# Kernel optimization log

Hardware: AMD Instinct MI355X
Metric: run time of the kernel (lower is better)

Reference implementation:

```python
import jax, jax.numpy as jnp
import numpy as np

F_SIZE = 256
N_HEAD = 4
D_HEAD = F_SIZE // N_HEAD
B = 16384
E = 31  # number of 'other' entities


def setup_inputs() -> dict:
    key = jax.random.key(0)
    ks = jax.random.split(key, 9)
    s = 1.0 / np.sqrt(F_SIZE)  # ~ nn.Linear init scale
    inp = {
        "ego": jax.random.normal(ks[0], (B, 1, F_SIZE), dtype=jnp.float32),
        "others": jax.random.normal(ks[1], (B, E, F_SIZE), dtype=jnp.float32),
        "mask": jax.random.randint(ks[2], (B, E + 1), 0, 2).astype(bool),
        "Wq": jax.random.uniform(ks[3], (F_SIZE, F_SIZE), jnp.float32, -s, s),
        "Wk": jax.random.uniform(ks[4], (F_SIZE, F_SIZE), jnp.float32, -s, s),
        "Wv": jax.random.uniform(ks[5], (F_SIZE, F_SIZE), jnp.float32, -s, s),
        "Wok": jax.random.uniform(ks[6], (F_SIZE, F_SIZE), jnp.float32, -s, s),
        "Wov": jax.random.uniform(ks[7], (F_SIZE, F_SIZE), jnp.float32, -s, s),
        "Wc": jax.random.uniform(ks[8], (F_SIZE, F_SIZE), jnp.float32, -s, s),
    }
    return inp


def reference(ego, others, mask, Wq, Wk, Wv, Wok, Wov, Wc):
    b = others.shape[0]
    e = others.shape[1]
    # nn.Linear(bias=False): y = x @ W.T
    ego_q = (ego @ Wq.T).reshape(b, 1, N_HEAD, D_HEAD)
    ego_k = (ego @ Wk.T).reshape(b, 1, N_HEAD, D_HEAD)
    ego_v = (ego @ Wv.T).reshape(b, 1, N_HEAD, D_HEAD)
    oth_k = (others @ Wok.T).reshape(b, e, N_HEAD, D_HEAD)
    oth_v = (others @ Wov.T).reshape(b, e, N_HEAD, D_HEAD)
    all_k = jnp.concatenate([ego_k, oth_k], axis=1)  # (b, e+1, h, d)
    all_v = jnp.concatenate([ego_v, oth_v], axis=1)
    # scores: single query per head -> (b, h, 1, e+1)
    scores = jnp.einsum('bqhd,bkhd->bhqk', ego_q, all_k) / np.sqrt(D_HEAD)
    scores = jnp.where(mask[:, None, None, :], jnp.float32(-1e9), scores)
    attn = jax.nn.softmax(scores, axis=-1)
    value = jnp.einsum('bhqk,bkhd->bqhd', attn, all_v).reshape(b, F_SIZE)
    res = ((value @ Wc.T) + ego[:, 0, :]) * 0.5
    return res, attn
```

## Files before the change

### kernel.cpp

```cpp
#include <hip/hip_runtime.h>
#include <hip/hip_bf16.h>

typedef __attribute__((ext_vector_type(8))) short bf16x8;
typedef __attribute__((ext_vector_type(4))) float f32x4;

#define NB 16384
#define NE 31

static __device__ __forceinline__ unsigned short f2b(float f) {
  unsigned int u = __builtin_bit_cast(unsigned int, f);
  return (unsigned short)((u + 0x7fffu + ((u >> 16) & 1u)) >> 16);
}
static __device__ __forceinline__ float b2f(unsigned short h) {
  return __builtin_bit_cast(float, ((unsigned int)h) << 16);
}


__global__ void k0_base(const float* __restrict__ wq, const float* __restrict__ wk,
                        const float* __restrict__ wv, const float* __restrict__ wc,
                        unsigned short* __restrict__ W1, unsigned short* __restrict__ W2) {
  int r = blockIdx.x, k = threadIdx.x;
  if (r < 256) {
    W1[r * 256 + k] = f2b(0.125f * wq[r * 256 + k]);
  } else if (r < 512) {
    W1[r * 256 + k] = f2b(wk[(r - 256) * 256 + k]);
  } else if (r < 768) {
    W1[r * 256 + k] = f2b(wv[(r - 512) * 256 + k]);
  } else {
    int n = r - 768;
    W2[n * 1280 + 1024 + k] = f2b(wc[n * 256 + k]);
  }
}

__global__ void k0_wqo(const float* __restrict__ wq, const float* __restrict__ wok,
                       unsigned short* __restrict__ W1) {
  int m = blockIdx.x;
  int k = threadIdx.x;
  int h = m >> 8, c = m & 255;
  float acc = 0.f;
#pragma unroll 8
  for (int d = 0; d < 64; ++d)
    acc = fmaf(wq[(h * 64 + d) * 256 + k], wok[(h * 64 + d) * 256 + c], acc);
  W1[(768 + m) * 256 + k] = f2b(0.125f * acc);
}

__global__ void k0_g(const float* __restrict__ wov, const float* __restrict__ wc,
                     unsigned short* __restrict__ W2) {
  int n = blockIdx.x;
  int t = threadIdx.x;
#pragma unroll 1
  for (int mi = 0; mi < 4; ++mi) {
    float acc = 0.f;
#pragma unroll 8
    for (int d = 0; d < 64; ++d)
      acc = fmaf(wov[(mi * 64 + d) * 256 + t], wc[n * 256 + mi * 64 + d], acc);
    W2[n * 1280 + mi * 256 + t] = f2b(acc);
  }
}

__global__ __launch_bounds__(256, 2)
void k1b(const float* __restrict__ ego, const unsigned short* __restrict__ W1,
         unsigned short* __restrict__ qkv2) {
  __shared__ __align__(16) unsigned short Al[64 * 256];
  const int tid = threadIdx.x;
  const int bM = blockIdx.x * 64;
#pragma unroll
  for (int it = 0; it < 8; ++it) {
    int c = tid + it * 256;
    int row = c >> 5, k8 = c & 31;
    const float4* g = (const float4*)(ego + (size_t)(bM + row) * 256 + k8 * 8);
    float4 x = g[0], y = g[1];
    float t[8] = {x.x, x.y, x.z, x.w, y.x, y.y, y.z, y.w};
    bf16x8 v;
#pragma unroll
    for (int j = 0; j < 8; ++j) v[j] = (short)f2b(t[j]);
    int byteoff = row * 512 + ((k8 * 16) ^ ((row & 7) << 4));
    *(bf16x8*)((char*)Al + byteoff) = v;
  }
  __syncthreads();
  const int w = tid >> 6, lane = tid & 63, lr = lane & 15, lkg = lane >> 4;
#pragma unroll 1
  for (int cb = 0; cb < 7; ++cb) {
    int bN = w * 448 + cb * 64;
    f32x4 acc[4][4];
#pragma unroll
    for (int mt = 0; mt < 4; ++mt)
#pragma unroll
      for (int nt = 0; nt < 4; ++nt) acc[mt][nt] = (f32x4){0.f, 0.f, 0.f, 0.f};
#pragma unroll
    for (int kk = 0; kk < 8; ++kk) {
      int kidx = kk * 32 + lkg * 8;
      bf16x8 bfr[4];
#pragma unroll
      for (int nt = 0; nt < 4; ++nt)
        bfr[nt] = *(const bf16x8*)(W1 + (size_t)(bN + nt * 16 + lr) * 256 + kidx);
#pragma unroll
      for (int mt = 0; mt < 4; ++mt) {
        int row = mt * 16 + lr;
        int byteoff = row * 512 + ((kidx * 2) ^ ((row & 7) << 4));
        bf16x8 a = *(const bf16x8*)((const char*)Al + byteoff);
#pragma unroll
        for (int nt = 0; nt < 4; ++nt)
          acc[mt][nt] = __builtin_amdgcn_mfma_f32_16x16x32_bf16(a, bfr[nt], acc[mt][nt], 0, 0, 0);
      }
    }
#pragma unroll
    for (int mt = 0; mt < 4; ++mt)
#pragma unroll
      for (int nt = 0; nt < 4; ++nt)
#pragma unroll
        for (int j = 0; j < 4; ++j) {
          int row = bM + mt * 16 + lkg * 4 + j;
          int col = bN + nt * 16 + lr;
          qkv2[(size_t)row * 1792 + col] = f2b(acc[mt][nt][j]);
        }
  }
}

__global__ __launch_bounds__(256, 4)
void ks_attn(const float* __restrict__ others, const int* __restrict__ mask,
             const unsigned short* __restrict__ qkv2,
             unsigned short* __restrict__ u,
             float* __restrict__ attnout) {
  __shared__ __align__(16) unsigned short Xr[32 * 264];
  __shared__ __align__(16) unsigned short Qo_l[1024];
  __shared__ __align__(16) unsigned short qk_l[768];
  __shared__ float sco_l[4][32];
  __shared__ float Pl[4][32];
  const int tid = threadIdx.x;
  const size_t b = blockIdx.x;

  {
    int e = tid >> 3, c = tid & 7;
    if (e < 31) {
      const float4* src = (const float4*)(others) + ((b * 31 + e) * 64 + c * 8);
      float4 f[8];
#pragma unroll
      for (int j = 0; j < 8; ++j) f[j] = src[j];
#pragma unroll
      for (int j = 0; j < 4; ++j) {
        bf16x8 v;
        v[0] = (short)f2b(f[2 * j].x);     v[1] = (short)f2b(f[2 * j].y);
        v[2] = (short)f2b(f[2 * j].z);     v[3] = (short)f2b(f[2 * j].w);
        v[4] = (short)f2b(f[2 * j + 1].x); v[5] = (short)f2b(f[2 * j + 1].y);
        v[6] = (short)f2b(f[2 * j + 1].z); v[7] = (short)f2b(f[2 * j + 1].w);
        *(bf16x8*)(&Xr[e * 264 + c * 32 + j * 8]) = v;
      }
    } else {
      bf16x8 z = (bf16x8){0, 0, 0, 0, 0, 0, 0, 0};
#pragma unroll
      for (int j = 0; j < 4; ++j) *(bf16x8*)(&Xr[31 * 264 + c * 32 + j * 8]) = z;
    }
    if (tid < 224) {
      bf16x8 v = *(const bf16x8*)(qkv2 + b * 1792 + tid * 8);
      if (tid < 96) *(bf16x8*)(&qk_l[tid * 8]) = v;
      else          *(bf16x8*)(&Qo_l[(tid - 96) * 8]) = v;
    }
  }
  __syncthreads();

  const int w = tid >> 6, lane = tid & 63, lr = lane & 15, lkg = lane >> 4;

  if (w < 2) {
    f32x4 acc = (f32x4){0.f, 0.f, 0.f, 0.f};
#pragma unroll
    for (int kk = 0; kk < 8; ++kk) {
      bf16x8 a = *(const bf16x8*)(&Qo_l[(lr & 3) * 256 + kk * 32 + lkg * 8]);
      bf16x8 bb = *(const bf16x8*)(&Xr[(w * 16 + lr) * 264 + kk * 32 + lkg * 8]);
      acc = __builtin_amdgcn_mfma_f32_16x16x32_bf16(a, bb, acc, 0, 0, 0);
    }
    if (lkg == 0) {
      int n = w * 16 + lr;
      if (n < NE) {
#pragma unroll
        for (int j = 0; j < 4; ++j) sco_l[j][1 + n] = acc[j];
      }
    }
  } else if (w == 2) {
    int h = lane >> 4, i = lane & 15;
    const unsigned short* q4 = &qk_l[h * 64 + i * 4];
    const unsigned short* k4p = &qk_l[256 + h * 64 + i * 4];
    float s = 0.f;
#pragma unroll
    for (int j = 0; j < 4; ++j) s += b2f(q4[j]) * b2f(k4p[j]);
#pragma unroll
    for (int off = 1; off < 16; off <<= 1) s += __shfl_xor(s, off, 16);
    if (i == 0) sco_l[h][0] = s;
  }
  __syncthreads();

  {
    int key = lane & 31;
    float s = sco_l[w][key];
    if (mask[b * 32 + key] != 0) s = -1e9f;
    float mx = s;
#pragma unroll
    for (int off = 1; off < 32; off <<= 1) mx = fmaxf(mx, __shfl_xor(mx, off, 32));
    float ex = __expf(s - mx);
    float sm = ex;
#pragma unroll
    for (int off = 1; off < 32; off <<= 1) sm += __shfl_xor(sm, off, 32);
    float p = ex / sm;
    if (lane < 32) {
      Pl[w][key] = p;
      attnout[b * 128 + w * 32 + key] = p;
    }
  }

  {
    float a0 = 0.f, a1 = 0.f, a2 = 0.f, a3 = 0.f;
#pragma unroll
    for (int e = 0; e < NE; ++e) {
      float p = Pl[w][1 + e];
      ushort4 xv = *(const ushort4*)(&Xr[e * 264 + lane * 4]);
      a0 = fmaf(p, b2f(xv.x), a0);
      a1 = fmaf(p, b2f(xv.y), a1);
      a2 = fmaf(p, b2f(xv.z), a2);
      a3 = fmaf(p, b2f(xv.w), a3);
    }
    ushort4 st;
    st.x = f2b(a0); st.y = f2b(a1); st.z = f2b(a2); st.w = f2b(a3);
    *(ushort4*)(u + b * 1280 + w * 256 + lane * 4) = st;
    float p0 = Pl[w][0];
    u[b * 1280 + 1024 + w * 64 + lane] = f2b(p0 * b2f(qk_l[512 + w * 64 + lane]));
  }
}

__global__ __launch_bounds__(256, 2)
void k4_out(const unsigned short* __restrict__ u, const unsigned short* __restrict__ W2,
            const float* __restrict__ ego, float* __restrict__ out) {
  __shared__ __align__(16) unsigned short Au[32 * 256];
  const int tid = threadIdx.x;
  const int bM = blockIdx.x * 32;
  const int w = tid >> 6, lane = tid & 63, lr = lane & 15, lkg = lane >> 4;
  f32x4 acc[2][4];
#pragma unroll
  for (int mt = 0; mt < 2; ++mt)
#pragma unroll
    for (int nt = 0; nt < 4; ++nt) acc[mt][nt] = (f32x4){0.f, 0.f, 0.f, 0.f};
#pragma unroll 1
  for (int kc = 0; kc < 5; ++kc) {
#pragma unroll
    for (int it = 0; it < 4; ++it) {
      int c = tid + it * 256;
      int row = c >> 5, k8 = c & 31;
      bf16x8 v = *(const bf16x8*)(u + (size_t)(bM + row) * 1280 + kc * 256 + k8 * 8);
      int byteoff = row * 512 + ((k8 * 16) ^ ((row & 7) << 4));
      *(bf16x8*)((char*)Au + byteoff) = v;
    }
    __syncthreads();
#pragma unroll
    for (int kk = 0; kk < 8; ++kk) {
      int kidx = kk * 32 + lkg * 8;
      bf16x8 bfr[4];
#pragma unroll
      for (int nt = 0; nt < 4; ++nt)
        bfr[nt] = *(const bf16x8*)(W2 + (size_t)(w * 64 + nt * 16 + lr) * 1280 + kc * 256 + kidx);
#pragma unroll
      for (int mt = 0; mt < 2; ++mt) {
        int row = mt * 16 + lr;
        int byteoff = row * 512 + ((kidx * 2) ^ ((row & 7) << 4));
        bf16x8 a = *(const bf16x8*)((const char*)Au + byteoff);
#pragma unroll
        for (int nt = 0; nt < 4; ++nt)
          acc[mt][nt] = __builtin_amdgcn_mfma_f32_16x16x32_bf16(a, bfr[nt], acc[mt][nt], 0, 0, 0);
      }
    }
    __syncthreads();
  }
#pragma unroll
  for (int mt = 0; mt < 2; ++mt)
#pragma unroll
    for (int nt = 0; nt < 4; ++nt)
#pragma unroll
      for (int j = 0; j < 4; ++j) {
        int row = bM + mt * 16 + lkg * 4 + j;
        int col = w * 64 + nt * 16 + lr;
        out[(size_t)row * 256 + col] = (acc[mt][nt][j] + ego[(size_t)row * 256 + col]) * 0.5f;
      }
}

extern "C" void kernel_launch(void* const* d_in, const int* in_sizes, int n_in,
                              void* d_out, int out_size, void* d_ws, size_t ws_size,
                              hipStream_t stream) {
  const float* ego    = (const float*)d_in[0];
  const float* others = (const float*)d_in[1];
  const int*   mask   = (const int*)d_in[2];
  const float* wq  = (const float*)d_in[3];
  const float* wk  = (const float*)d_in[4];
  const float* wv  = (const float*)d_in[5];
  const float* wok = (const float*)d_in[6];
  const float* wov = (const float*)d_in[7];
  const float* wc  = (const float*)d_in[8];

  unsigned short* W1   = (unsigned short*)d_ws;
  unsigned short* W2   = W1 + 1792 * 256;
  unsigned short* qkv2 = W2 + 256 * 1280;
  unsigned short* u    = qkv2 + (size_t)NB * 1792;

  float* res  = (float*)d_out;
  float* attn = res + (size_t)NB * 256;

  hipLaunchKernelGGL(k0_base, dim3(1024), dim3(256), 0, stream, wq, wk, wv, wc, W1, W2);
  hipLaunchKernelGGL(k0_wqo,  dim3(1024), dim3(256), 0, stream, wq, wok, W1);
  hipLaunchKernelGGL(k0_g,    dim3(256),  dim3(256), 0, stream, wov, wc, W2);
  hipLaunchKernelGGL(k1b,     dim3(256),  dim3(256), 0, stream, ego, W1, qkv2);
  hipLaunchKernelGGL(ks_attn, dim3(NB),   dim3(256), 0, stream, others, mask, qkv2, u, attn);
  hipLaunchKernelGGL(k4_out,  dim3(512),  dim3(256), 0, stream, u, W2, ego, res);
}
```

Baseline: 268.1 us.

## Make attention kernel persistent with register-prefetched next batch and merge weight-prep kernels

The attention kernel now runs on a fixed grid of 1024 blocks. Each block loops over 16 batch rows and issues global loads for the next row into registers while computing the current one. The mask is staged in shared memory, and the three weight-preparation kernels are merged into one launch. The aim is to hide the global-load latency of the dominant memory-bound kernel and to cut launch overhead. In exchange, register pressure rises from holding the prefetch buffers, each iteration needs an extra barrier, and fewer blocks are resident to hide latency.

```diff
diff --git a/kernel.cpp b/kernel.cpp
--- a/kernel.cpp
+++ b/kernel.cpp
@@ -6,6 +6,8 @@
 
 #define NB 16384
 #define NE 31
+#define KS_GRID 1024
+#define KS_ITEMS (NB / KS_GRID)
 
 static __device__ __forceinline__ unsigned short f2b(float f) {
   unsigned int u = __builtin_bit_cast(unsigned int, f);
@@ -15,46 +17,40 @@
   return __builtin_bit_cast(float, ((unsigned int)h) << 16);
 }
 
-
-__global__ void k0_base(const float* __restrict__ wq, const float* __restrict__ wk,
-                        const float* __restrict__ wv, const float* __restrict__ wc,
-                        unsigned short* __restrict__ W1, unsigned short* __restrict__ W2) {
+__global__ void k0_all(const float* __restrict__ wq, const float* __restrict__ wk,
+                       const float* __restrict__ wv, const float* __restrict__ wok,
+                       const float* __restrict__ wov, const float* __restrict__ wc,
+                       unsigned short* __restrict__ W1, unsigned short* __restrict__ W2) {
   int r = blockIdx.x, k = threadIdx.x;
-  if (r < 256) {
-    W1[r * 256 + k] = f2b(0.125f * wq[r * 256 + k]);
-  } else if (r < 512) {
-    W1[r * 256 + k] = f2b(wk[(r - 256) * 256 + k]);
-  } else if (r < 768) {
-    W1[r * 256 + k] = f2b(wv[(r - 512) * 256 + k]);
-  } else {
-    int n = r - 768;
-    W2[n * 1280 + 1024 + k] = f2b(wc[n * 256 + k]);
-  }
-}
-
-__global__ void k0_wqo(const float* __restrict__ wq, const float* __restrict__ wok,
-                       unsigned short* __restrict__ W1) {
-  int m = blockIdx.x;
-  int k = threadIdx.x;
-  int h = m >> 8, c = m & 255;
-  float acc = 0.f;
-#pragma unroll 8
-  for (int d = 0; d < 64; ++d)
-    acc = fmaf(wq[(h * 64 + d) * 256 + k], wok[(h * 64 + d) * 256 + c], acc);
-  W1[(768 + m) * 256 + k] = f2b(0.125f * acc);
-}
-
-__global__ void k0_g(const float* __restrict__ wov, const float* __restrict__ wc,
-                     unsigned short* __restrict__ W2) {
-  int n = blockIdx.x;
-  int t = threadIdx.x;
-#pragma unroll 1
-  for (int mi = 0; mi < 4; ++mi) {
+  if (r < 1024) {
+    if (r < 256) {
+      W1[r * 256 + k] = f2b(0.125f * wq[r * 256 + k]);
+    } else if (r < 512) {
+      W1[r * 256 + k] = f2b(wk[(r - 256) * 256 + k]);
+    } else if (r < 768) {
+      W1[r * 256 + k] = f2b(wv[(r - 512) * 256 + k]);
+    } else {
+      int n = r - 768;
+      W2[n * 1280 + 1024 + k] = f2b(wc[n * 256 + k]);
+    }
+  } else if (r < 2048) {
+    int m = r - 1024;
+    int h = m >> 8, c = m & 255;
     float acc = 0.f;
 #pragma unroll 8
     for (int d = 0; d < 64; ++d)
-      acc = fmaf(wov[(mi * 64 + d) * 256 + t], wc[n * 256 + mi * 64 + d], acc);
-    W2[n * 1280 + mi * 256 + t] = f2b(acc);
+      acc = fmaf(wq[(h * 64 + d) * 256 + k], wok[(h * 64 + d) * 256 + c], acc);
+    W1[(768 + m) * 256 + k] = f2b(0.125f * acc);
+  } else {
+    int n = r - 2048;
+#pragma unroll 1
+    for (int mi = 0; mi < 4; ++mi) {
+      float acc = 0.f;
+#pragma unroll 8
+      for (int d = 0; d < 64; ++d)
+        acc = fmaf(wov[(mi * 64 + d) * 256 + k], wc[n * 256 + mi * 64 + d], acc);
+      W2[n * 1280 + mi * 256 + k] = f2b(acc);
+    }
   }
 }
 
@@ -125,18 +121,29 @@
   __shared__ __align__(16) unsigned short Xr[32 * 264];
   __shared__ __align__(16) unsigned short Qo_l[1024];
   __shared__ __align__(16) unsigned short qk_l[768];
+  __shared__ int maskl[32];
   __shared__ float sco_l[4][32];
   __shared__ float Pl[4][32];
   const int tid = threadIdx.x;
-  const size_t b = blockIdx.x;
-
-  {
-    int e = tid >> 3, c = tid & 7;
+  const int w = tid >> 6, lane = tid & 63, lr = lane & 15, lkg = lane >> 4;
+  const int e = tid >> 3, c = tid & 7;
+  const size_t b0 = (size_t)blockIdx.x * KS_ITEMS;
+
+  float4 f[8];
+  bf16x8 qv;
+  int4 mv;
+
+  auto issue = [&](size_t bb) {
     if (e < 31) {
-      const float4* src = (const float4*)(others) + ((b * 31 + e) * 64 + c * 8);
-      float4 f[8];
+      const float4* src = (const float4*)(others) + ((bb * 31 + e) * 64 + c * 8);
 #pragma unroll
       for (int j = 0; j < 8; ++j) f[j] = src[j];
+    }
+    if (tid < 224) qv = *(const bf16x8*)(qkv2 + bb * 1792 + tid * 8);
+    if (tid >= 248) mv = *(const int4*)(mask + bb * 32 + (tid - 248) * 4);
+  };
+  auto commit = [&]() {
+    if (e < 31) {
 #pragma unroll
       for (int j = 0; j < 4; ++j) {
         bf16x8 v;
@@ -150,79 +157,90 @@
       bf16x8 z = (bf16x8){0, 0, 0, 0, 0, 0, 0, 0};
 #pragma unroll
       for (int j = 0; j < 4; ++j) *(bf16x8*)(&Xr[31 * 264 + c * 32 + j * 8]) = z;
+      *(int4*)(&maskl[(tid - 248) * 4]) = mv;
     }
     if (tid < 224) {
-      bf16x8 v = *(const bf16x8*)(qkv2 + b * 1792 + tid * 8);
-      if (tid < 96) *(bf16x8*)(&qk_l[tid * 8]) = v;
-      else          *(bf16x8*)(&Qo_l[(tid - 96) * 8]) = v;
-    }
-  }
-  __syncthreads();
-
-  const int w = tid >> 6, lane = tid & 63, lr = lane & 15, lkg = lane >> 4;
-
-  if (w < 2) {
-    f32x4 acc = (f32x4){0.f, 0.f, 0.f, 0.f};
-#pragma unroll
-    for (int kk = 0; kk < 8; ++kk) {
-      bf16x8 a = *(const bf16x8*)(&Qo_l[(lr & 3) * 256 + kk * 32 + lkg * 8]);
-      bf16x8 bb = *(const bf16x8*)(&Xr[(w * 16 + lr) * 264 + kk * 32 + lkg * 8]);
-      acc = __builtin_amdgcn_mfma_f32_16x16x32_bf16(a, bb, acc, 0, 0, 0);
-    }
-    if (lkg == 0) {
-      int n = w * 16 + lr;
-      if (n < NE) {
-#pragma unroll
-        for (int j = 0; j < 4; ++j) sco_l[j][1 + n] = acc[j];
-      }
-    }
-  } else if (w == 2) {
-    int h = lane >> 4, i = lane & 15;
-    const unsigned short* q4 = &qk_l[h * 64 + i * 4];
-    const unsigned short* k4p = &qk_l[256 + h * 64 + i * 4];
-    float s = 0.f;
-#pragma unroll
-    for (int j = 0; j < 4; ++j) s += b2f(q4[j]) * b2f(k4p[j]);
-#pragma unroll
-    for (int off = 1; off < 16; off <<= 1) s += __shfl_xor(s, off, 16);
-    if (i == 0) sco_l[h][0] = s;
-  }
-  __syncthreads();
-
-  {
-    int key = lane & 31;
-    float s = sco_l[w][key];
-    if (mask[b * 32 + key] != 0) s = -1e9f;
-    float mx = s;
-#pragma unroll
-    for (int off = 1; off < 32; off <<= 1) mx = fmaxf(mx, __shfl_xor(mx, off, 32));
-    float ex = __expf(s - mx);
-    float sm = ex;
-#pragma unroll
-    for (int off = 1; off < 32; off <<= 1) sm += __shfl_xor(sm, off, 32);
-    float p = ex / sm;
-    if (lane < 32) {
-      Pl[w][key] = p;
-      attnout[b * 128 + w * 32 + key] = p;
-    }
-  }
-
-  {
-    float a0 = 0.f, a1 = 0.f, a2 = 0.f, a3 = 0.f;
-#pragma unroll
-    for (int e = 0; e < NE; ++e) {
-      float p = Pl[w][1 + e];
-      ushort4 xv = *(const ushort4*)(&Xr[e * 264 + lane * 4]);
-      a0 = fmaf(p, b2f(xv.x), a0);
-      a1 = fmaf(p, b2f(xv.y), a1);
-      a2 = fmaf(p, b2f(xv.z), a2);
-      a3 = fmaf(p, b2f(xv.w), a3);
-    }
-    ushort4 st;
-    st.x = f2b(a0); st.y = f2b(a1); st.z = f2b(a2); st.w = f2b(a3);
-    *(ushort4*)(u + b * 1280 + w * 256 + lane * 4) = st;
-    float p0 = Pl[w][0];
-    u[b * 1280 + 1024 + w * 64 + lane] = f2b(p0 * b2f(qk_l[512 + w * 64 + lane]));
+      if (tid < 96) *(bf16x8*)(&qk_l[tid * 8]) = qv;
+      else          *(bf16x8*)(&Qo_l[(tid - 96) * 8]) = qv;
+    }
+  };
+
+  issue(b0);
+#pragma unroll 1
+  for (int it = 0; it < KS_ITEMS; ++it) {
+    const size_t bb = b0 + it;
+    commit();
+    if (it + 1 < KS_ITEMS) issue(bb + 1);
+    asm volatile("s_waitcnt lgkmcnt(0)" ::: "memory");
+    __builtin_amdgcn_s_barrier();
+
+    if (w < 2) {
+      f32x4 acc = (f32x4){0.f, 0.f, 0.f, 0.f};
+#pragma unroll
+      for (int kk = 0; kk < 8; ++kk) {
+        bf16x8 a = *(const bf16x8*)(&Qo_l[(lr & 3) * 256 + kk * 32 + lkg * 8]);
+        bf16x8 bbf = *(const bf16x8*)(&Xr[(w * 16 + lr) * 264 + kk * 32 + lkg * 8]);
+        acc = __builtin_amdgcn_mfma_f32_16x16x32_bf16(a, bbf, acc, 0, 0, 0);
+      }
+      if (lkg == 0) {
+        int n = w * 16 + lr;
+        if (n < NE) {
+#pragma unroll
+          for (int j = 0; j < 4; ++j) sco_l[j][1 + n] = acc[j];
+        }
+      }
+    } else if (w == 2) {
+      int h = lane >> 4, i = lane & 15;
+      const unsigned short* q4 = &qk_l[h * 64 + i * 4];
+      const unsigned short* k4p = &qk_l[256 + h * 64 + i * 4];
+      float s = 0.f;
+#pragma unroll
+      for (int j = 0; j < 4; ++j) s += b2f(q4[j]) * b2f(k4p[j]);
+#pragma unroll
+      for (int off = 1; off < 16; off <<= 1) s += __shfl_xor(s, off, 16);
+      if (i == 0) sco_l[h][0] = s;
+    }
+    asm volatile("s_waitcnt lgkmcnt(0)" ::: "memory");
+    __builtin_amdgcn_s_barrier();
+
+    {
+      int key = lane & 31;
+      float s = sco_l[w][key];
+      if (maskl[key] != 0) s = -1e9f;
+      float mx = s;
+#pragma unroll
+      for (int off = 1; off < 32; off <<= 1) mx = fmaxf(mx, __shfl_xor(mx, off, 32));
+      float ex = __expf(s - mx);
+      float sm = ex;
+#pragma unroll
+      for (int off = 1; off < 32; off <<= 1) sm += __shfl_xor(sm, off, 32);
+      float p = ex / sm;
+      if (lane < 32) {
+        Pl[w][key] = p;
+        attnout[bb * 128 + w * 32 + key] = p;
+      }
+    }
+
+    {
+      float a0 = 0.f, a1 = 0.f, a2 = 0.f, a3 = 0.f;
+#pragma unroll
+      for (int ee = 0; ee < NE; ++ee) {
+        float p = Pl[w][1 + ee];
+        ushort4 xv = *(const ushort4*)(&Xr[ee * 264 + lane * 4]);
+        a0 = fmaf(p, b2f(xv.x), a0);
+        a1 = fmaf(p, b2f(xv.y), a1);
+        a2 = fmaf(p, b2f(xv.z), a2);
+        a3 = fmaf(p, b2f(xv.w), a3);
+      }
+      ushort4 st;
+      st.x = f2b(a0); st.y = f2b(a1); st.z = f2b(a2); st.w = f2b(a3);
+      *(ushort4*)(u + bb * 1280 + w * 256 + lane * 4) = st;
+      float p0 = Pl[w][0];
+      u[bb * 1280 + 1024 + w * 64 + lane] = f2b(p0 * b2f(qk_l[512 + w * 64 + lane]));
+    }
+    asm volatile("" ::: "memory");
+    __builtin_amdgcn_s_barrier();
+    asm volatile("" ::: "memory");
   }
 }
 
@@ -301,10 +319,10 @@
   float* res  = (float*)d_out;
   float* attn = res + (size_t)NB * 256;
 
-  hipLaunchKernelGGL(k0_base, dim3(1024), dim3(256), 0, stream, wq, wk, wv, wc, W1, W2);
-  hipLaunchKernelGGL(k0_wqo,  dim3(1024), dim3(256), 0, stream, wq, wok, W1);
-  hipLaunchKernelGGL(k0_g,    dim3(256),  dim3(256), 0, stream, wov, wc, W2);
-  hipLaunchKernelGGL(k1b,     dim3(256),  dim3(256), 0, stream, ego, W1, qkv2);
-  hipLaunchKernelGGL(ks_attn, dim3(NB),   dim3(256), 0, stream, others, mask, qkv2, u, attn);
-  hipLaunchKernelGGL(k4_out,  dim3(512),  dim3(256), 0, stream, u, W2, ego, res);
-}
+  hipLaunchKernelGGL(k0_all, dim3(2304), dim3(256), 0, stream,
+                     wq, wk, wv, wok, wov, wc, W1, W2);
+  hipLaunchKernelGGL(k1b,    dim3(256),  dim3(256), 0, stream, ego, W1, qkv2);
+  hipLaunchKernelGGL(ks_attn, dim3(KS_GRID), dim3(256), 0, stream,
+                     others, mask, qkv2, u, attn);
+  hipLaunchKernelGGL(k4_out, dim3(512),  dim3(256), 0, stream, u, W2, ego, res);
+}
```

Result: slower. 528.5 us (+97.1%).
